# Optimization experiments

Measured on AMD Instinct MI355X. Metric: run time of the kernel, lower is better.

Reference implementation:

```python
import jax, jax.numpy as jnp
import numpy as np

INF = 1.0e9
B, NI, NJ = 1, 768, 768
C_NODE, C_PAIR = 512, 128
H, C_HID = 8, 32
LN_EPS = 1e-5


def _ln(x, w, b):
    m = jnp.mean(x, axis=-1, keepdims=True)
    v = jnp.mean(jnp.square(x - m), axis=-1, keepdims=True)
    return (x - m) * jax.lax.rsqrt(v + LN_EPS) * w + b


def setup_inputs() -> dict:
    key = jax.random.key(0)
    ks = jax.random.split(key, 16)
    s_node = 1.0 / np.sqrt(C_NODE)
    s_pair = 1.0 / np.sqrt(C_PAIR)
    s_hid = 1.0 / np.sqrt(H * C_HID)
    inp = {
        "node_embed_i": jax.random.normal(ks[0], (B, NI, C_NODE), jnp.float32),
        "node_embed_j": jax.random.normal(ks[1], (B, NJ, C_NODE), jnp.float32),
        "pair_embed": jax.random.normal(ks[2], (B, NI, NJ, C_PAIR), jnp.float32),
        "pair_mask": (jax.random.uniform(ks[3], (B, NI, NJ)) < 0.95).astype(jnp.float32),
        "node_mask_i": (jax.random.uniform(ks[4], (B, NI)) < 0.98).astype(jnp.float32),
        # LayerNorm params
        "ln_i_w": jnp.ones((C_NODE,), jnp.float32), "ln_i_b": jnp.zeros((C_NODE,), jnp.float32),
        "ln_j_w": jnp.ones((C_NODE,), jnp.float32), "ln_j_b": jnp.zeros((C_NODE,), jnp.float32),
        "ln_p_w": jnp.ones((C_PAIR,), jnp.float32), "ln_p_b": jnp.zeros((C_PAIR,), jnp.float32),
        # pair-bias projection and its gate: Linear(C_PAIR, H)
        "W_pb": jax.random.normal(ks[5], (C_PAIR, H), jnp.float32) * s_pair,
        "b_pb": jnp.zeros((H,), jnp.float32),
        "W_pg": jax.random.normal(ks[6], (C_PAIR, H), jnp.float32) * s_pair,
        "b_pg": jnp.zeros((H,), jnp.float32),
        # attention projections (q/k/v bias-free, OpenFold-style)
        "Wq": jax.random.normal(ks[7], (C_NODE, H * C_HID), jnp.float32) * s_node,
        "Wk": jax.random.normal(ks[8], (C_NODE, H * C_HID), jnp.float32) * s_node,
        "Wv": jax.random.normal(ks[9], (C_NODE, H * C_HID), jnp.float32) * s_node,
        # output gate and output projection
        "Wg": jax.random.normal(ks[10], (C_NODE, H * C_HID), jnp.float32) * s_node,
        "bg": jnp.zeros((H * C_HID,), jnp.float32),
        "Wo": jax.random.normal(ks[11], (H * C_HID, C_NODE), jnp.float32) * s_hid,
        "bo": jnp.zeros((C_NODE,), jnp.float32),
    }
    return inp


def reference(node_embed_i, node_embed_j, pair_embed, pair_mask, node_mask_i,
              ln_i_w, ln_i_b, ln_j_w, ln_j_b, ln_p_w, ln_p_b,
              W_pb, b_pb, W_pg, b_pg, Wq, Wk, Wv, Wg, bg, Wo, bo):
    # LayerNorms
    qx = _ln(node_embed_i, ln_i_w, ln_i_b)           # [B,NI,C_NODE]
    kx = _ln(node_embed_j, ln_j_w, ln_j_b)           # [B,NJ,C_NODE]
    p = _ln(pair_embed, ln_p_w, ln_p_b)              # [B,NI,NJ,C_PAIR]

    # additive mask bias: 0 where valid, -inf where masked; broadcast over heads
    mask_bias = (INF * (pair_mask - 1.0))[:, None, :, :]          # [B,1,NI,NJ]

    # gated pair bias -> [B,H,NI,NJ] (permute_final_dims([2,0,1]))
    pb = (p @ W_pb + b_pb) * jax.nn.sigmoid(p @ W_pg + b_pg)      # [B,NI,NJ,H]
    pair_bias = jnp.transpose(pb, (0, 3, 1, 2))

    # multi-head attention with injected biases
    q = (qx @ Wq).reshape(B, NI, H, C_HID) * (C_HID ** -0.5)
    k = (kx @ Wk).reshape(B, NJ, H, C_HID)
    v = (kx @ Wv).reshape(B, NJ, H, C_HID)
    scores = jnp.einsum('bihc,bjhc->bhij', q, k) + mask_bias + pair_bias
    a = jax.nn.softmax(scores, axis=-1)                           # [B,H,NI,NJ]
    o = jnp.einsum('bhij,bjhc->bihc', a, v)                       # [B,NI,H,C_HID]

    # sigmoid output gate, flatten heads, output projection
    g = jax.nn.sigmoid(qx @ Wg + bg).reshape(B, NI, H, C_HID)
    o = (o * g).reshape(B, NI, H * C_HID)
    mha_out = o @ Wo + bo                                         # [B,NI,C_NODE]

    # residual on the layernormed input, scaled by node mask (dropout = identity at inference)
    return qx + mha_out * node_mask_i[..., None]
```

## Files before the change

### kernel.cpp

```cpp
#include <hip/hip_runtime.h>
#include <hip/hip_bf16.h>

#define NI 768
#define NJ 768
#define CN 512
#define CP 128
#define NH 8
#define CH 32
#define HC 256
#define NSTR 6
#define SJ 128

typedef float  fx4  __attribute__((ext_vector_type(4)));
typedef float  fx2  __attribute__((ext_vector_type(2)));
typedef short  bv8  __attribute__((ext_vector_type(8)));
typedef unsigned short usx4 __attribute__((ext_vector_type(4)));

__device__ __forceinline__ short f2bf(float f) {
    __hip_bfloat16 h = __float2bfloat16(f);
    return *reinterpret_cast<short*>(&h);
}
__device__ __forceinline__ float bf2f(unsigned short u) {
    union { unsigned int u; float f; } c; c.u = ((unsigned int)u) << 16; return c.f;
}

__global__ __launch_bounds__(256) void fused_front_kernel(
    const float* __restrict__ node_i, const float* __restrict__ node_j,
    const float* __restrict__ ln_i_w, const float* __restrict__ ln_i_b,
    const float* __restrict__ ln_j_w, const float* __restrict__ ln_j_b,
    const float* __restrict__ Wq, const float* __restrict__ Wk,
    const float* __restrict__ Wv, const float* __restrict__ Wg,
    const float* __restrict__ bg,
    const float* __restrict__ lnpw, const float* __restrict__ lnpb,
    const float* __restrict__ Wpb, const float* __restrict__ bpb,
    const float* __restrict__ Wpg, const float* __restrict__ bpg,
    const float* __restrict__ pair, const float* __restrict__ pmask,
    float* __restrict__ qx, unsigned short* __restrict__ qsb,
    unsigned short* __restrict__ ksb, unsigned short* __restrict__ vtb,
    float* __restrict__ gs, unsigned short* __restrict__ biasb)
{
    const int bid = blockIdx.x;
    const int t = threadIdx.x;
    if (bid < 192) {
        __shared__ float xs[8][CN];
        __shared__ float red[4][8][2];
        const bool isj = bid >= 96;
        const int r0 = (isj ? bid - 96 : bid) * 8;
        const float* xin = isj ? node_j : node_i;
        const float* lw = isj ? ln_j_w : ln_i_w;
        const float* lb = isj ? ln_j_b : ln_i_b;
        const int wv = t >> 6;

        fx2 vrow[8]; float s8[8], q8[8];
#pragma unroll
        for (int r = 0; r < 8; ++r) {
            vrow[r] = *(const fx2*)(xin + (size_t)(r0 + r) * CN + t * 2);
            s8[r] = vrow[r][0] + vrow[r][1];
            q8[r] = vrow[r][0] * vrow[r][0] + vrow[r][1] * vrow[r][1];
        }
#pragma unroll
        for (int d = 1; d < 64; d <<= 1)
#pragma unroll
            for (int r = 0; r < 8; ++r) {
                s8[r] += __shfl_xor(s8[r], d);
                q8[r] += __shfl_xor(q8[r], d);
            }
        if ((t & 63) == 0)
#pragma unroll
            for (int r = 0; r < 8; ++r) { red[wv][r][0] = s8[r]; red[wv][r][1] = q8[r]; }
        __syncthreads();
        fx2 lwv = *(const fx2*)(lw + t * 2), lbv = *(const fx2*)(lb + t * 2);
#pragma unroll
        for (int r = 0; r < 8; ++r) {
            float s = red[0][r][0] + red[1][r][0] + red[2][r][0] + red[3][r][0];
            float q = red[0][r][1] + red[1][r][1] + red[2][r][1] + red[3][r][1];
            float mean = s * (1.f / CN);
            float var = q * (1.f / CN) - mean * mean;
            float rs = rsqrtf(var + 1e-5f);
            fx2 o;
            o[0] = (vrow[r][0] - mean) * rs * lwv[0] + lbv[0];
            o[1] = (vrow[r][1] - mean) * rs * lwv[1] + lbv[1];
            xs[r][t * 2] = o[0]; xs[r][t * 2 + 1] = o[1];
            if (!isj) *(fx2*)(qx + (size_t)(r0 + r) * CN + t * 2) = o;
        }
        __syncthreads();

        for (int m = 0; m < 2; ++m) {
            const float* W = isj ? (m ? Wv : Wk) : (m ? Wg : Wq);
            float acc[8] = {0.f,0.f,0.f,0.f,0.f,0.f,0.f,0.f};
            for (int cc = 0; cc < CN; cc += 4) {
                fx4 xv[8];
#pragma unroll
                for (int r = 0; r < 8; ++r) xv[r] = *(const fx4*)&xs[r][cc];
#pragma unroll
                for (int u = 0; u < 4; ++u) {
                    float w = W[(size_t)(cc + u) * HC + t];
#pragma unroll
                    for (int r = 0; r < 8; ++r) acc[r] = fmaf(xv[r][u], w, acc[r]);
                }
            }
            if (!isj) {
                if (m == 0) {
#pragma unroll
                    for (int r = 0; r < 8; ++r)
                        qsb[(size_t)(r0 + r) * HC + t] =
                            (unsigned short)f2bf(acc[r] * 0.17677669529663687f);
                } else {
#pragma unroll
                    for (int r = 0; r < 8; ++r)
                        gs[(size_t)(r0 + r) * HC + t] =
                            1.f / (1.f + __expf(-(acc[r] + bg[t])));
                }
            } else {
                if (m == 0) {
#pragma unroll
                    for (int r = 0; r < 8; ++r)
                        ksb[(size_t)(r0 + r) * HC + t] = (unsigned short)f2bf(acc[r]);
                } else {
                    bv8 vv;
#pragma unroll
                    for (int r = 0; r < 8; ++r) vv[r] = f2bf(acc[r]);
                    *(bv8*)&vtb[(size_t)t * NJ + r0] = vv;
                }
            }
        }
        return;
    }

    __shared__ unsigned short wcatT[16][136];
    __shared__ float redS[16][16], redC[16][16];
    __shared__ float scalS[16], scalC[16];
    __shared__ unsigned short sb[8][68];

    const int lane = t & 63;
    const int wave = t >> 6;
    const int bid2 = bid - 192;
    const int i    = bid2 / 12;
    const int jt64 = (bid2 % 12) * 64;
    const int jt   = jt64 + wave * 16;
    const int o  = lane & 15;
    const int kq = lane >> 4;

    const float* prow = pair + ((size_t)i * NJ + (jt + o)) * CP + kq * 8;
    fx4 x0[4], x1[4];
#pragma unroll
    for (int s = 0; s < 4; ++s) {
        x0[s] = *(const fx4*)(prow + s * 32);
        x1[s] = *(const fx4*)(prow + s * 32 + 4);
    }

    {
        const int oo = t & 15, cg = t >> 4;
        float pS = 0.f, pC = 0.f;
#pragma unroll
        for (int e = 0; e < 8; ++e) {
            int c = cg * 8 + e;
            float w = (oo < 8) ? Wpb[c * 8 + oo] : Wpg[c * 8 + (oo - 8)];
            float wv = lnpw[c] * w;
            short b = f2bf(wv);
            wcatT[oo][c] = (unsigned short)b;
            pS += bf2f((unsigned short)b);
            pC += lnpb[c] * w;
        }
        redS[cg][oo] = pS; redC[cg][oo] = pC;
        __syncthreads();
        if (t < 16) {
            float s = 0.f, c2 = 0.f;
#pragma unroll
            for (int k = 0; k < 16; ++k) { s += redS[k][t]; c2 += redC[k][t]; }
            scalS[t] = s;
            scalC[t] = c2 + ((t < 8) ? bpb[t] : bpg[t - 8]);
        }
        __syncthreads();
    }

    bv8 bfrag[4];
#pragma unroll
    for (int s = 0; s < 4; ++s)
        bfrag[s] = *(const bv8*)&wcatT[o][s * 32 + kq * 8];
    const float spb = scalS[o];
    const float cpb = scalC[o];

    bv8 afrag[4];
#pragma unroll
    for (int s = 0; s < 4; ++s) {
#pragma unroll
        for (int u = 0; u < 4; ++u) {
            afrag[s][u]     = f2bf(x0[s][u]);
            afrag[s][u + 4] = f2bf(x1[s][u]);
        }
    }
    bv8 ones;
#pragma unroll
    for (int u = 0; u < 8; ++u) ones[u] = (short)0x3F80;

    fx4 acc  = {0.f, 0.f, 0.f, 0.f};
    fx4 accS = {0.f, 0.f, 0.f, 0.f};
    fx4 accG = {0.f, 0.f, 0.f, 0.f};
#pragma unroll
    for (int s = 0; s < 4; ++s) {
        acc  = __builtin_amdgcn_mfma_f32_16x16x32_bf16(afrag[s], bfrag[s], acc,  0, 0, 0);
        accS = __builtin_amdgcn_mfma_f32_16x16x32_bf16(afrag[s], ones,     accS, 0, 0, 0);
        accG = __builtin_amdgcn_mfma_f32_16x16x32_bf16(afrag[s], afrag[s], accG, 0, 0, 0);
    }

#pragma unroll
    for (int r = 0; r < 4; ++r) {
        const int p = kq * 4 + r;
        float sp = accS[r];
        float qp = __shfl(accG[r], kq * 20 + r);
        float mean = sp * (1.f / CP);
        float var  = qp * (1.f / CP) - mean * mean;
        float rstd = rsqrtf(var + 1e-5f);
        float pre  = rstd * (acc[r] - mean * spb) + cpb;
        float part = __shfl_xor(pre, 8);
        if (o < 8) {
            float sig = 1.f / (1.f + __expf(-part));
            int j = jt + p;
            float b = pre * sig + (pmask[(size_t)i * NJ + j] - 1.f) * 1.0e9f;
            sb[o][wave * 16 + p] = (unsigned short)f2bf(b);
        }
    }
    __syncthreads();
    if (t < 128) {
        const int oo = t >> 4, ck = t & 15;
        usx4 v;
#pragma unroll
        for (int u = 0; u < 4; ++u) v[u] = sb[oo][ck * 4 + u];
        *(usx4*)&biasb[((size_t)oo * NI + i) * NJ + jt64 + ck * 4] = v;
    }
}

__global__ __launch_bounds__(256) void attn_kernel(
    const short* __restrict__ qsb, const short* __restrict__ ksb,
    const short* __restrict__ vtb, const unsigned short* __restrict__ biasb,
    float* __restrict__ pnum, float* __restrict__ pden)
{
    __shared__ unsigned short P[32][136];
    __shared__ float sumbuf[4][32];
    const int i0 = blockIdx.x * 32;
    const int h  = blockIdx.y;
    const int jbase = blockIdx.z * SJ;
    const int pb = ((int)blockIdx.x * NH + h) * NSTR + blockIdx.z;
    const int t = threadIdx.x;
    const int w = t >> 6;
    const int lane = t & 63;
    const int rowl = lane & 15;
    const int g = lane >> 4;

    bv8 aq[2];
#pragma unroll
    for (int it = 0; it < 2; ++it)
        aq[it] = *(const bv8*)&qsb[(size_t)(i0 + it * 16 + rowl) * HC + h * CH + g * 8];

    bv8 bk[2];
#pragma unroll
    for (int jt = 0; jt < 2; ++jt) {
        const int jb = jbase + w * 32 + jt * 16;
        bk[jt] = *(const bv8*)&ksb[(size_t)(jb + rowl) * HC + h * CH + g * 8];
    }
    const unsigned short* bbase = biasb + (size_t)h * NI * NJ;
    unsigned short bl[2][2][4];
#pragma unroll
    for (int jt = 0; jt < 2; ++jt) {
        const int jb = jbase + w * 32 + jt * 16;
#pragma unroll
        for (int it = 0; it < 2; ++it)
#pragma unroll
            for (int r = 0; r < 4; ++r) {
                const int il = it * 16 + g * 4 + r;
                bl[jt][it][r] = bbase[(size_t)(i0 + il) * NJ + jb + rowl];
            }
    }

    float rs[2][4] = {{0.f,0.f,0.f,0.f},{0.f,0.f,0.f,0.f}};
#pragma unroll
    for (int jt = 0; jt < 2; ++jt) {
        const int jloc = w * 32 + jt * 16;
#pragma unroll
        for (int it = 0; it < 2; ++it) {
            fx4 acc = {0.f, 0.f, 0.f, 0.f};
            acc = __builtin_amdgcn_mfma_f32_16x16x32_bf16(aq[it], bk[jt], acc, 0, 0, 0);
#pragma unroll
            for (int r = 0; r < 4; ++r) {
                const int il = it * 16 + g * 4 + r;
                float s = acc[r] + bf2f(bl[jt][it][r]);
                float p = __expf(s);
                rs[it][r] += p;
                P[il][jloc + rowl] = (unsigned short)f2bf(p);
            }
        }
    }
#pragma unroll
    for (int it = 0; it < 2; ++it)
#pragma unroll
        for (int r = 0; r < 4; ++r) {
            float v = rs[it][r];
            v += __shfl_xor(v, 1); v += __shfl_xor(v, 2);
            v += __shfl_xor(v, 4); v += __shfl_xor(v, 8);
            rs[it][r] = v;
        }
    if (rowl == 0) {
#pragma unroll
        for (int it = 0; it < 2; ++it)
#pragma unroll
            for (int r = 0; r < 4; ++r)
                sumbuf[w][it * 16 + g * 4 + r] = rs[it][r];
    }

    const int it = w & 1, ct = w >> 1;
    bv8 vv[4];
#pragma unroll
    for (int kk = 0; kk < 4; ++kk)
        vv[kk] = *(const bv8*)&vtb[(size_t)(h * CH + ct * 16 + rowl) * NJ + jbase + kk * 32 + g * 8];

    __syncthreads();

    if (t < 32)
        pden[(size_t)pb * 32 + t] =
            sumbuf[0][t] + sumbuf[1][t] + sumbuf[2][t] + sumbuf[3][t];

    fx4 acc = {0.f, 0.f, 0.f, 0.f};
#pragma unroll
    for (int kk = 0; kk < 4; ++kk) {
        bv8 ap = *(const bv8*)&P[it * 16 + rowl][kk * 32 + g * 8];
        acc = __builtin_amdgcn_mfma_f32_16x16x32_bf16(ap, vv[kk], acc, 0, 0, 0);
    }
#pragma unroll
    for (int r = 0; r < 4; ++r) {
        const int il = it * 16 + g * 4 + r;
        pnum[(size_t)pb * 1024 + il * 32 + ct * 16 + rowl] = acc[r];
    }
}

__global__ __launch_bounds__(256) void combine_out_kernel(
    const float* __restrict__ pnum, const float* __restrict__ pden,
    const float* __restrict__ gs, const float* __restrict__ qx,
    const float* __restrict__ Wo, const float* __restrict__ bo,
    const float* __restrict__ mi, float* __restrict__ outp)
{
    __shared__ float ogl[2][HC];
    const int r0 = blockIdx.x * 2;
    const int t = threadIdx.x;
    const int h = t >> 5, c = t & 31;
#pragma unroll
    for (int r = 0; r < 2; ++r) {
        const int i = r0 + r;
        const int pb = ((i >> 5) * NH + h) * NSTR;
        const int il = i & 31;
        float n = 0.f, d = 0.f;
#pragma unroll
        for (int s = 0; s < NSTR; ++s) {
            n += pnum[(size_t)(pb + s) * 1024 + il * 32 + c];
            d += pden[(size_t)(pb + s) * 32 + il];
        }
        ogl[r][t] = n / d * gs[(size_t)i * HC + t];
    }
    __syncthreads();

    float acc[2][2] = {{0,0},{0,0}};
    for (int cc = 0; cc < HC; cc += 4) {
        fx4 xr0 = *(const fx4*)&ogl[0][cc];
        fx4 xr1 = *(const fx4*)&ogl[1][cc];
#pragma unroll
        for (int u = 0; u < 4; ++u) {
            float w0 = Wo[(size_t)(cc + u) * CN + t];
            float w1 = Wo[(size_t)(cc + u) * CN + 256 + t];
            acc[0][0] = fmaf(xr0[u], w0, acc[0][0]); acc[0][1] = fmaf(xr0[u], w1, acc[0][1]);
            acc[1][0] = fmaf(xr1[u], w0, acc[1][0]); acc[1][1] = fmaf(xr1[u], w1, acc[1][1]);
        }
    }
#pragma unroll
    for (int r = 0; r < 2; ++r) {
        float mk = mi[r0 + r];
        size_t base = (size_t)(r0 + r) * CN;
        outp[base + t]       = qx[base + t]       + (acc[r][0] + bo[t])       * mk;
        outp[base + 256 + t] = qx[base + 256 + t] + (acc[r][1] + bo[t + 256]) * mk;
    }
}

extern "C" void kernel_launch(void* const* d_in, const int* in_sizes, int n_in,
                              void* d_out, int out_size, void* d_ws, size_t ws_size,
                              hipStream_t stream)
{
    const float* node_i = (const float*)d_in[0];
    const float* node_j = (const float*)d_in[1];
    const float* pair   = (const float*)d_in[2];
    const float* pmask  = (const float*)d_in[3];
    const float* nmask  = (const float*)d_in[4];
    const float* ln_i_w = (const float*)d_in[5];
    const float* ln_i_b = (const float*)d_in[6];
    const float* ln_j_w = (const float*)d_in[7];
    const float* ln_j_b = (const float*)d_in[8];
    const float* ln_p_w = (const float*)d_in[9];
    const float* ln_p_b = (const float*)d_in[10];
    const float* W_pb   = (const float*)d_in[11];
    const float* b_pb   = (const float*)d_in[12];
    const float* W_pg   = (const float*)d_in[13];
    const float* b_pg   = (const float*)d_in[14];
    const float* Wq     = (const float*)d_in[15];
    const float* Wk     = (const float*)d_in[16];
    const float* Wv     = (const float*)d_in[17];
    const float* Wg     = (const float*)d_in[18];
    const float* bg     = (const float*)d_in[19];
    const float* Wo     = (const float*)d_in[20];
    const float* bo     = (const float*)d_in[21];
    float* outp = (float*)d_out;

    float* fw = (float*)d_ws;
    float* qx   = fw;
    float* gs   = qx + (size_t)NI * CN;
    float* pnum = gs + (size_t)NI * HC;
    float* pden = pnum + (size_t)24 * NH * NSTR * 1024;
    unsigned short* qsb = (unsigned short*)(pden + (size_t)24 * NH * NSTR * 32);
    unsigned short* ksb = qsb + (size_t)NI * HC;
    unsigned short* vtb = ksb + (size_t)NJ * HC;
    unsigned short* biasb = vtb + (size_t)HC * NJ;

    hipLaunchKernelGGL(fused_front_kernel, dim3(192 + (NI * NJ) / 64), dim3(256), 0, stream,
                       node_i, node_j, ln_i_w, ln_i_b, ln_j_w, ln_j_b,
                       Wq, Wk, Wv, Wg, bg,
                       ln_p_w, ln_p_b, W_pb, b_pb, W_pg, b_pg,
                       pair, pmask,
                       qx, qsb, ksb, vtb, gs, biasb);
    hipLaunchKernelGGL(attn_kernel, dim3(NI / 32, NH, NSTR), dim3(256), 0, stream,
                       (const short*)qsb, (const short*)ksb, (const short*)vtb,
                       biasb, pnum, pden);
    hipLaunchKernelGGL(combine_out_kernel, dim3(NI / 2), dim3(256), 0, stream,
                       pnum, pden, gs, qx, Wo, bo, nmask, outp);
}
```

Before: 110.0 us.

## Process four pair tiles per block with double-buffered register prefetch

The pair-bias part of the front kernel now has each block handle 256 j positions instead of 64, so the per-block weight transpose and reduction setup is amortised over four tiles. Pair rows for the next tile are loaded into registers while the current tile goes through its MFMAs, which overlaps global loads with compute. The mask row is staged in shared memory and the bias is written out with wider 8-element stores. In exchange the grid is four times smaller and each thread holds more registers, which may lower occupancy.

```diff
diff --git a/kernel.cpp b/kernel.cpp
--- a/kernel.cpp
+++ b/kernel.cpp
@@ -14,7 +14,7 @@
 typedef float  fx4  __attribute__((ext_vector_type(4)));
 typedef float  fx2  __attribute__((ext_vector_type(2)));
 typedef short  bv8  __attribute__((ext_vector_type(8)));
-typedef unsigned short usx4 __attribute__((ext_vector_type(4)));
+typedef unsigned short usx8 __attribute__((ext_vector_type(8)));
 
 __device__ __forceinline__ short f2bf(float f) {
     __hip_bfloat16 h = __float2bfloat16(f);
@@ -130,24 +130,32 @@
     __shared__ unsigned short wcatT[16][136];
     __shared__ float redS[16][16], redC[16][16];
     __shared__ float scalS[16], scalC[16];
-    __shared__ unsigned short sb[8][68];
+    __shared__ float pm[256];
+    __shared__ unsigned short sb[8][256];
 
     const int lane = t & 63;
     const int wave = t >> 6;
     const int bid2 = bid - 192;
-    const int i    = bid2 / 12;
-    const int jt64 = (bid2 % 12) * 64;
-    const int jt   = jt64 + wave * 16;
+    const int i    = bid2 / 3;
+    const int jq   = bid2 % 3;
     const int o  = lane & 15;
     const int kq = lane >> 4;
 
-    const float* prow = pair + ((size_t)i * NJ + (jt + o)) * CP + kq * 8;
-    fx4 x0[4], x1[4];
-#pragma unroll
-    for (int s = 0; s < 4; ++s) {
-        x0[s] = *(const fx4*)(prow + s * 32);
-        x1[s] = *(const fx4*)(prow + s * 32 + 4);
-    }
+    const float* pbase = pair + ((size_t)i * NJ + jq * 256 + wave * 16 + o) * CP + kq * 8;
+
+    fx4 xa0[4], xa1[4], xb0[4], xb1[4];
+    auto loadp = [&](fx4* px0, fx4* px1, int tt) {
+        const float* pr = pbase + (size_t)tt * 64 * CP;
+#pragma unroll
+        for (int s = 0; s < 4; ++s) {
+            px0[s] = *(const fx4*)(pr + s * 32);
+            px1[s] = *(const fx4*)(pr + s * 32 + 4);
+        }
+    };
+
+    loadp(xa0, xa1, 0);
+    if (t < 64)
+        *(fx4*)&pm[t * 4] = *(const fx4*)&pmask[(size_t)i * NJ + jq * 256 + t * 4];
 
     {
         const int oo = t & 15, cg = t >> 4;
@@ -181,53 +189,63 @@
     const float spb = scalS[o];
     const float cpb = scalC[o];
 
-    bv8 afrag[4];
-#pragma unroll
-    for (int s = 0; s < 4; ++s) {
-#pragma unroll
-        for (int u = 0; u < 4; ++u) {
-            afrag[s][u]     = f2bf(x0[s][u]);
-            afrag[s][u + 4] = f2bf(x1[s][u]);
-        }
-    }
     bv8 ones;
 #pragma unroll
     for (int u = 0; u < 8; ++u) ones[u] = (short)0x3F80;
 
-    fx4 acc  = {0.f, 0.f, 0.f, 0.f};
-    fx4 accS = {0.f, 0.f, 0.f, 0.f};
-    fx4 accG = {0.f, 0.f, 0.f, 0.f};
-#pragma unroll
-    for (int s = 0; s < 4; ++s) {
-        acc  = __builtin_amdgcn_mfma_f32_16x16x32_bf16(afrag[s], bfrag[s], acc,  0, 0, 0);
-        accS = __builtin_amdgcn_mfma_f32_16x16x32_bf16(afrag[s], ones,     accS, 0, 0, 0);
-        accG = __builtin_amdgcn_mfma_f32_16x16x32_bf16(afrag[s], afrag[s], accG, 0, 0, 0);
-    }
-
-#pragma unroll
-    for (int r = 0; r < 4; ++r) {
-        const int p = kq * 4 + r;
-        float sp = accS[r];
-        float qp = __shfl(accG[r], kq * 20 + r);
-        float mean = sp * (1.f / CP);
-        float var  = qp * (1.f / CP) - mean * mean;
-        float rstd = rsqrtf(var + 1e-5f);
-        float pre  = rstd * (acc[r] - mean * spb) + cpb;
-        float part = __shfl_xor(pre, 8);
-        if (o < 8) {
-            float sig = 1.f / (1.f + __expf(-part));
-            int j = jt + p;
-            float b = pre * sig + (pmask[(size_t)i * NJ + j] - 1.f) * 1.0e9f;
-            sb[o][wave * 16 + p] = (unsigned short)f2bf(b);
-        }
-    }
+    auto process = [&](const fx4* px0, const fx4* px1, int tt) {
+        bv8 afrag[4];
+#pragma unroll
+        for (int s = 0; s < 4; ++s) {
+#pragma unroll
+            for (int u = 0; u < 4; ++u) {
+                afrag[s][u]     = f2bf(px0[s][u]);
+                afrag[s][u + 4] = f2bf(px1[s][u]);
+            }
+        }
+        fx4 acc  = {0.f, 0.f, 0.f, 0.f};
+        fx4 accS = {0.f, 0.f, 0.f, 0.f};
+        fx4 accG = {0.f, 0.f, 0.f, 0.f};
+#pragma unroll
+        for (int s = 0; s < 4; ++s) {
+            acc  = __builtin_amdgcn_mfma_f32_16x16x32_bf16(afrag[s], bfrag[s], acc,  0, 0, 0);
+            accS = __builtin_amdgcn_mfma_f32_16x16x32_bf16(afrag[s], ones,     accS, 0, 0, 0);
+            accG = __builtin_amdgcn_mfma_f32_16x16x32_bf16(afrag[s], afrag[s], accG, 0, 0, 0);
+        }
+#pragma unroll
+        for (int r = 0; r < 4; ++r) {
+            const int p = kq * 4 + r;
+            float sp = accS[r];
+            float qp = __shfl(accG[r], kq * 20 + r);
+            float mean = sp * (1.f / CP);
+            float var  = qp * (1.f / CP) - mean * mean;
+            float rstd = rsqrtf(var + 1e-5f);
+            float pre  = rstd * (acc[r] - mean * spb) + cpb;
+            float part = __shfl_xor(pre, 8);
+            if (o < 8) {
+                float sig = 1.f / (1.f + __expf(-part));
+                const int jl = tt * 64 + wave * 16 + p;
+                float b = pre * sig + (pm[jl] - 1.f) * 1.0e9f;
+                sb[o][jl] = (unsigned short)f2bf(b);
+            }
+        }
+    };
+
+    loadp(xb0, xb1, 1);
+    process(xa0, xa1, 0);
+    loadp(xa0, xa1, 2);
+    process(xb0, xb1, 1);
+    loadp(xb0, xb1, 3);
+    process(xa0, xa1, 2);
+    process(xb0, xb1, 3);
+
     __syncthreads();
-    if (t < 128) {
-        const int oo = t >> 4, ck = t & 15;
-        usx4 v;
-#pragma unroll
-        for (int u = 0; u < 4; ++u) v[u] = sb[oo][ck * 4 + u];
-        *(usx4*)&biasb[((size_t)oo * NI + i) * NJ + jt64 + ck * 4] = v;
+    {
+        const int oo = t >> 5, ck = t & 31;
+        usx8 v;
+#pragma unroll
+        for (int u = 0; u < 8; ++u) v[u] = sb[oo][ck * 8 + u];
+        *(usx8*)&biasb[((size_t)oo * NI + i) * NJ + jq * 256 + ck * 8] = v;
     }
 }
 
@@ -417,7 +435,7 @@
     unsigned short* vtb = ksb + (size_t)NJ * HC;
     unsigned short* biasb = vtb + (size_t)HC * NJ;
 
-    hipLaunchKernelGGL(fused_front_kernel, dim3(192 + (NI * NJ) / 64), dim3(256), 0, stream,
+    hipLaunchKernelGGL(fused_front_kernel, dim3(192 + NI * 3), dim3(256), 0, stream,
                        node_i, node_j, ln_i_w, ln_i_b, ln_j_w, ln_j_b,
                        Wq, Wk, Wv, Wg, bg,
                        ln_p_w, ln_p_b, W_pb, b_pb, W_pg, b_pg,
```

After: 115.4 us. 4.9% more time.
